# Kernel tuning notes

Measured on AMD Instinct MI355X. Metric: run time of the kernel, lower is better.

Reference implementation:

```python
import jax, jax.numpy as jnp
import numpy as np

NUM_EXPERTS = 8
TOP_K = 2


def setup_inputs() -> dict:
    key = jax.random.key(0)
    k1, k2, k3, k4, k5 = jax.random.split(key, 5)
    B, S, H, F, E = 4, 2048, 1024, 4096, NUM_EXPERTS
    return {
        "hidden_states": jax.random.normal(k1, (B, S, H), dtype=jnp.float32),
        "gate_w": jax.random.normal(k2, (E, H), dtype=jnp.float32) * 0.02,
        "w1": jax.random.normal(k3, (E, F, H), dtype=jnp.float32) * 0.02,
        "w3": jax.random.normal(k4, (E, F, H), dtype=jnp.float32) * 0.02,
        "w2": jax.random.normal(k5, (E, H, F), dtype=jnp.float32) * 0.02,
    }


def reference(hidden_states, gate_w, w1, w3, w2):
    B, S, H = hidden_states.shape
    E = gate_w.shape[0]
    x = hidden_states.reshape(-1, H)  # [T, H]
    T = x.shape[0]

    # Router: logits -> fp32 softmax -> top-k -> renormalize (Mixtral)
    router_logits = x @ gate_w.T  # [T, E]
    probs = jax.nn.softmax(router_logits.astype(jnp.float32), axis=-1)
    top_w, top_idx = jax.lax.top_k(probs, TOP_K)  # [T, K]
    top_w = top_w / jnp.sum(top_w, axis=-1, keepdims=True)
    top_w = top_w.astype(x.dtype)

    # Combine weights per (token, expert); zero for unselected experts.
    comb = jnp.zeros((T, E), dtype=x.dtype).at[
        jnp.arange(T)[:, None], top_idx
    ].add(top_w)  # [T, E]

    out = jnp.zeros((T, H), dtype=x.dtype)
    for e in range(E):  # structural loop over distinct expert weights
        h = jax.nn.silu(x @ w1[e].T) * (x @ w3[e].T)  # [T, F]
        out = out + comb[:, e:e + 1] * (h @ w2[e].T)  # [T, H]

    return out.reshape(B, S, H), router_logits
```

## Files before the change

kernel.cpp:

```cpp
#include <hip/hip_runtime.h>
#include <hip/hip_bf16.h>
#include <stdint.h>

#define T_TOK 8192
#define H_DIM 1024
#define F_DIM 4096
#define NEXP  8
#define CAP        17408
#define CAP_TILES  136

typedef __attribute__((ext_vector_type(8))) short bf16x8;
typedef __attribute__((ext_vector_type(4))) float f32x4;

#define AS1 __attribute__((address_space(1)))
#define AS3 __attribute__((address_space(3)))

__device__ __forceinline__ void gload_lds16(const void* g, void* l) {
  __builtin_amdgcn_global_load_lds((const AS1 void*)g, (AS3 void*)l, 16, 0, 0);
}

struct TK { int i0, i1; float w0, w1; };

__global__ __launch_bounds__(256) void router_kernel(
    const float* __restrict__ x, const float* __restrict__ gw,
    float* __restrict__ logits, int* __restrict__ counts, TK* __restrict__ tk)
{
  const int lane = threadIdx.x & 63;
  const int t = blockIdx.x * 4 + (threadIdx.x >> 6);
  const float* xp = x + (size_t)t * H_DIM;
  float xr[16];
#pragma unroll
  for (int i = 0; i < 16; ++i) xr[i] = xp[lane + i * 64];
  float lg[NEXP];
#pragma unroll
  for (int e = 0; e < NEXP; ++e) {
    const float* gp = gw + e * H_DIM;
    float acc = 0.f;
#pragma unroll
    for (int i = 0; i < 16; ++i) acc += xr[i] * gp[lane + i * 64];
#pragma unroll
    for (int s = 32; s > 0; s >>= 1) acc += __shfl_xor(acc, s, 64);
    lg[e] = acc;
  }
  if (lane < NEXP) logits[(size_t)t * NEXP + lane] = lg[lane];
  if (lane == 0) {
    int i0 = 0; float m0 = lg[0];
#pragma unroll
    for (int e = 1; e < NEXP; ++e) if (lg[e] > m0) { m0 = lg[e]; i0 = e; }
    int i1 = -1; float m1 = -1e30f;
#pragma unroll
    for (int e = 0; e < NEXP; ++e) if (e != i0 && lg[e] > m1) { m1 = lg[e]; i1 = e; }
    float r = expf(m1 - m0);
    float w0 = 1.f / (1.f + r);
    float w1 = r / (1.f + r);
    TK v; v.i0 = i0; v.i1 = i1; v.w0 = w0; v.w1 = w1;
    tk[t] = v;
    atomicAdd(&counts[i0], 1);
    atomicAdd(&counts[i1], 1);
  }
}

__global__ __launch_bounds__(256) void scan_kernel(
    const int* __restrict__ counts, int* __restrict__ offs,
    int* __restrict__ cursor, int* __restrict__ tile_expert)
{
  __shared__ int so[NEXP + 1];
  const int tid = threadIdx.x;
  if (tid == 0) {
    int o = 0;
    for (int e = 0; e < NEXP; ++e) {
      so[e] = o; offs[e] = o; cursor[e] = o;
      o += (counts[e] + 127) & ~127;
    }
    so[NEXP] = o; offs[NEXP] = o;
  }
  __syncthreads();
  for (int ti = tid; ti < CAP_TILES; ti += 256) {
    int row = ti * 128;
    int e = NEXP - 1;
#pragma unroll
    for (int k = 0; k < NEXP; ++k)
      if (row >= so[k] && row < so[k + 1]) { e = k; break; }
    tile_expert[ti] = e;
  }
}

__global__ __launch_bounds__(256) void scatter_kernel(
    const TK* __restrict__ tk, int* __restrict__ cursor,
    int* __restrict__ pair_tok, float* __restrict__ pair_w,
    int2* __restrict__ inv)
{
  int t = blockIdx.x * 256 + threadIdx.x;
  if (t >= T_TOK) return;
  TK v = tk[t];
  int p0 = atomicAdd(&cursor[v.i0], 1);
  pair_tok[p0] = t; pair_w[p0] = v.w0;
  int p1 = atomicAdd(&cursor[v.i1], 1);
  pair_tok[p1] = t; pair_w[p1] = v.w1;
  inv[t] = make_int2(p0, p1);
}

union Pack8 { __hip_bfloat16 o[8]; uint4 u; };

__global__ __launch_bounds__(256) void gather_kernel(
    const float* __restrict__ x, const int* __restrict__ pair_tok,
    __hip_bfloat16* __restrict__ xg)
{
  int idx = blockIdx.x * 256 + threadIdx.x;
  int row = idx >> 7;
  int c8  = (idx & 127) << 3;
  int tok = pair_tok[row];
  const float4* src = reinterpret_cast<const float4*>(x + (size_t)tok * H_DIM + c8);
  float4 a = src[0], b = src[1];
  Pack8 pk;
  pk.o[0] = __float2bfloat16(a.x); pk.o[1] = __float2bfloat16(a.y);
  pk.o[2] = __float2bfloat16(a.z); pk.o[3] = __float2bfloat16(a.w);
  pk.o[4] = __float2bfloat16(b.x); pk.o[5] = __float2bfloat16(b.y);
  pk.o[6] = __float2bfloat16(b.z); pk.o[7] = __float2bfloat16(b.w);
  *reinterpret_cast<uint4*>(xg + (size_t)row * H_DIM + c8) = pk.u;
}

__global__ __launch_bounds__(256) void convert_kernel(
    const float* __restrict__ src, __hip_bfloat16* __restrict__ dst, long long n)
{
  long long i = ((long long)blockIdx.x * 256 + threadIdx.x) * 8;
  if (i >= n) return;
  float4 a = *reinterpret_cast<const float4*>(src + i);
  float4 b = *reinterpret_cast<const float4*>(src + i + 4);
  Pack8 pk;
  pk.o[0] = __float2bfloat16(a.x); pk.o[1] = __float2bfloat16(a.y);
  pk.o[2] = __float2bfloat16(a.z); pk.o[3] = __float2bfloat16(a.w);
  pk.o[4] = __float2bfloat16(b.x); pk.o[5] = __float2bfloat16(b.y);
  pk.o[6] = __float2bfloat16(b.z); pk.o[7] = __float2bfloat16(b.w);
  *reinterpret_cast<uint4*>(dst + i) = pk.u;
}


__global__ __launch_bounds__(256, 2) void gemm1_kernel(
    const __hip_bfloat16* __restrict__ xg,
    const __hip_bfloat16* __restrict__ w1b,
    const __hip_bfloat16* __restrict__ w3b,
    const int* __restrict__ tile_expert,
    __hip_bfloat16* __restrict__ h)
{
  __shared__ __hip_bfloat16 sA[128 * 32], sB1[128 * 32], sB3[128 * 32];
  const int n_ = blockIdx.x;
  const int swz = (n_ & 7) * 544 + (n_ >> 3);
  const int tf = swz & 31;
  const int tm = swz >> 5;
  const int e  = tile_expert[tm];
  const int tid = threadIdx.x;

  const __hip_bfloat16* A  = xg  + (size_t)tm * 128 * H_DIM;
  const __hip_bfloat16* B1 = w1b + (size_t)e * F_DIM * H_DIM + (size_t)tf * 128 * H_DIM;
  const __hip_bfloat16* B3 = w3b + (size_t)e * F_DIM * H_DIM + (size_t)tf * 128 * H_DIM;

  const int r     = tid >> 2;
  const int s_src = (tid & 3) ^ ((r >> 1) & 3);
  const int kc    = s_src * 8;
  const int lo    = tid * 8;

  f32x4 acc1[4][4] = {};
  f32x4 acc3[4][4] = {};

  const int wv = tid >> 6, lane = tid & 63;
  const int wr = wv >> 1, wc = wv & 1;
  const int l16 = lane & 15, lk = lane >> 4;
  const int rdk = (lk * 8) ^ (((l16 >> 1) & 3) * 8);

  for (int kt = 0; kt < H_DIM / 32; ++kt) {
    __syncthreads();
    const int gk = kt * 32 + kc;
    gload_lds16(A  + (size_t)r * H_DIM + gk,          &sA [lo]);
    gload_lds16(A  + (size_t)(r + 64) * H_DIM + gk,   &sA [2048 + lo]);
    gload_lds16(B1 + (size_t)r * H_DIM + gk,          &sB1[lo]);
    gload_lds16(B1 + (size_t)(r + 64) * H_DIM + gk,   &sB1[2048 + lo]);
    gload_lds16(B3 + (size_t)r * H_DIM + gk,          &sB3[lo]);
    gload_lds16(B3 + (size_t)(r + 64) * H_DIM + gk,   &sB3[2048 + lo]);
    __syncthreads();

    bf16x8 af[4], b1f[4], b3f[4];
#pragma unroll
    for (int m = 0; m < 4; ++m)
      af[m] = *reinterpret_cast<const bf16x8*>(&sA[(wr * 64 + m * 16 + l16) * 32 + rdk]);
#pragma unroll
    for (int n = 0; n < 4; ++n) {
      b1f[n] = *reinterpret_cast<const bf16x8*>(&sB1[(wc * 64 + n * 16 + l16) * 32 + rdk]);
      b3f[n] = *reinterpret_cast<const bf16x8*>(&sB3[(wc * 64 + n * 16 + l16) * 32 + rdk]);
    }
#pragma unroll
    for (int m = 0; m < 4; ++m)
#pragma unroll
      for (int n = 0; n < 4; ++n) {
        acc1[m][n] = __builtin_amdgcn_mfma_f32_16x16x32_bf16(af[m], b1f[n], acc1[m][n], 0, 0, 0);
        acc3[m][n] = __builtin_amdgcn_mfma_f32_16x16x32_bf16(af[m], b3f[n], acc3[m][n], 0, 0, 0);
      }
  }

  __hip_bfloat16* hp = h + (size_t)tm * 128 * F_DIM + (size_t)tf * 128;
#pragma unroll
  for (int m = 0; m < 4; ++m)
#pragma unroll
    for (int n = 0; n < 4; ++n)
#pragma unroll
      for (int j = 0; j < 4; ++j) {
        int row = wr * 64 + m * 16 + lk * 4 + j;
        int col = wc * 64 + n * 16 + l16;
        float c1 = acc1[m][n][j];
        float c3 = acc3[m][n][j];
        float s  = c1 / (1.f + expf(-c1));
        hp[(size_t)row * F_DIM + col] = __float2bfloat16(s * c3);
      }
}

__global__ __launch_bounds__(256, 2) void gemm2_kernel(
    const __hip_bfloat16* __restrict__ h,
    const __hip_bfloat16* __restrict__ w2b,
    const int* __restrict__ tile_expert,
    const float* __restrict__ pair_w,
    float* __restrict__ y)
{
  __shared__ __hip_bfloat16 sA[128 * 32], sB[128 * 32];
  const int n_ = blockIdx.x;
  const int swz = (n_ & 7) * 136 + (n_ >> 3);
  const int tn = swz & 7;
  const int tm = swz >> 3;
  const int e  = tile_expert[tm];
  const int tid = threadIdx.x;

  const __hip_bfloat16* A = h   + (size_t)tm * 128 * F_DIM;
  const __hip_bfloat16* B = w2b + (size_t)e * H_DIM * F_DIM + (size_t)tn * 128 * F_DIM;

  const int r     = tid >> 2;
  const int s_src = (tid & 3) ^ ((r >> 1) & 3);
  const int kc    = s_src * 8;
  const int lo    = tid * 8;

  f32x4 acc[4][4] = {};
  const int wv = tid >> 6, lane = tid & 63;
  const int wr = wv >> 1, wc = wv & 1;
  const int l16 = lane & 15, lk = lane >> 4;
  const int rdk = (lk * 8) ^ (((l16 >> 1) & 3) * 8);

  for (int kt = 0; kt < F_DIM / 32; ++kt) {
    __syncthreads();
    const int gk = kt * 32 + kc;
    gload_lds16(A + (size_t)r * F_DIM + gk,          &sA[lo]);
    gload_lds16(A + (size_t)(r + 64) * F_DIM + gk,   &sA[2048 + lo]);
    gload_lds16(B + (size_t)r * F_DIM + gk,          &sB[lo]);
    gload_lds16(B + (size_t)(r + 64) * F_DIM + gk,   &sB[2048 + lo]);
    __syncthreads();

    bf16x8 af[4], bf[4];
#pragma unroll
    for (int m = 0; m < 4; ++m)
      af[m] = *reinterpret_cast<const bf16x8*>(&sA[(wr * 64 + m * 16 + l16) * 32 + rdk]);
#pragma unroll
    for (int n = 0; n < 4; ++n)
      bf[n] = *reinterpret_cast<const bf16x8*>(&sB[(wc * 64 + n * 16 + l16) * 32 + rdk]);
#pragma unroll
    for (int m = 0; m < 4; ++m)
#pragma unroll
      for (int n = 0; n < 4; ++n)
        acc[m][n] = __builtin_amdgcn_mfma_f32_16x16x32_bf16(af[m], bf[n], acc[m][n], 0, 0, 0);
  }

#pragma unroll
  for (int m = 0; m < 4; ++m)
#pragma unroll
    for (int j = 0; j < 4; ++j) {
      int rowg = tm * 128 + wr * 64 + m * 16 + lk * 4 + j;
      float w = pair_w[rowg];
      float* op = y + (size_t)rowg * H_DIM + tn * 128 + wc * 64;
#pragma unroll
      for (int n = 0; n < 4; ++n)
        op[n * 16 + l16] = w * acc[m][n][j];
    }
}

__global__ __launch_bounds__(256) void combine_kernel(
    const float* __restrict__ y, const int2* __restrict__ inv,
    float* __restrict__ out)
{
  int idx = blockIdx.x * 256 + threadIdx.x;
  int t  = idx >> 8;
  int c  = (idx & 255) << 2;
  int2 p = inv[t];
  float4 a = *reinterpret_cast<const float4*>(y + (size_t)p.x * H_DIM + c);
  float4 b = *reinterpret_cast<const float4*>(y + (size_t)p.y * H_DIM + c);
  float4 o; o.x = a.x + b.x; o.y = a.y + b.y; o.z = a.z + b.z; o.w = a.w + b.w;
  *reinterpret_cast<float4*>(out + (size_t)t * H_DIM + c) = o;
}

#define WS_COUNTS   0
#define WS_CURSOR   32
#define WS_OFFS     64
#define WS_TILEEXP  128
#define WS_TK       1024
#define WS_PAIRTOK  132096
#define WS_PAIRW    201728
#define WS_ZERO_BYTES 271360
#define WS_INV      271360
#define WS_XG       336896ll
#define WS_W1       (WS_XG + 35651584ll)
#define WS_W3       (WS_W1 + 67108864ll)
#define WS_W2       (WS_W3 + 67108864ll)
#define WS_H        (WS_W2 + 67108864ll)
#define WS_Y        WS_XG

extern "C" void kernel_launch(void* const* d_in, const int* in_sizes, int n_in,
                              void* d_out, int out_size, void* d_ws, size_t ws_size,
                              hipStream_t stream) {
  const float* x  = (const float*)d_in[0];
  const float* gw = (const float*)d_in[1];
  const float* w1 = (const float*)d_in[2];
  const float* w3 = (const float*)d_in[3];
  const float* w2 = (const float*)d_in[4];
  float* out    = (float*)d_out;
  float* logits = out + (size_t)T_TOK * H_DIM;

  char* ws = (char*)d_ws;
  int*   counts   = (int*)(ws + WS_COUNTS);
  int*   cursor   = (int*)(ws + WS_CURSOR);
  int*   offs     = (int*)(ws + WS_OFFS);
  int*   tile_exp = (int*)(ws + WS_TILEEXP);
  TK*    tk       = (TK*)(ws + WS_TK);
  int*   pair_tok = (int*)(ws + WS_PAIRTOK);
  float* pair_w   = (float*)(ws + WS_PAIRW);
  int2*  inv      = (int2*)(ws + WS_INV);
  __hip_bfloat16* xg  = (__hip_bfloat16*)(ws + WS_XG);
  __hip_bfloat16* w1b = (__hip_bfloat16*)(ws + WS_W1);
  __hip_bfloat16* w3b = (__hip_bfloat16*)(ws + WS_W3);
  __hip_bfloat16* w2b = (__hip_bfloat16*)(ws + WS_W2);
  __hip_bfloat16* hbuf = (__hip_bfloat16*)(ws + WS_H);
  float* ybuf = (float*)(ws + WS_Y);

  hipMemsetAsync(d_ws, 0, WS_ZERO_BYTES, stream);

  const long long nW = (long long)NEXP * F_DIM * H_DIM;
  convert_kernel<<<16384, 256, 0, stream>>>(w1, w1b, nW);
  convert_kernel<<<16384, 256, 0, stream>>>(w3, w3b, nW);
  convert_kernel<<<16384, 256, 0, stream>>>(w2, w2b, nW);

  router_kernel<<<T_TOK / 4, 256, 0, stream>>>(x, gw, logits, counts, tk);
  scan_kernel<<<1, 256, 0, stream>>>(counts, offs, cursor, tile_exp);
  scatter_kernel<<<T_TOK / 256, 256, 0, stream>>>(tk, cursor, pair_tok, pair_w, inv);
  gather_kernel<<<(CAP * 128) / 256, 256, 0, stream>>>(x, pair_tok, xg);

  gemm1_kernel<<<CAP_TILES * (F_DIM / 128), 256, 0, stream>>>(
      xg, w1b, w3b, tile_exp, hbuf);
  gemm2_kernel<<<CAP_TILES * (H_DIM / 128), 256, 0, stream>>>(
      hbuf, w2b, tile_exp, pair_w, ybuf);
  combine_kernel<<<(T_TOK * H_DIM / 4) / 256, 256, 0, stream>>>(ybuf, inv, out);
}
```

Baseline: 1.011 ms.

## Use 256-row tiles, 512 threads, BK=64 double-buffered LDS in expert GEMMs

Both expert GEMMs move to 256x128 tiles with 8 waves, a K-step of 64, and double-buffered LDS. The next tile's global-to-LDS load is issued before the current tile's MFMAs, and s_setprio raises wave priority around the MFMA block. Expert capacity padding becomes 256-row multiples, so there is more padded work, but B reuse per tile doubles and each loop step needs one barrier instead of two. The larger LDS footprint (about 96 KB for gemm1) may limit occupancy.

After: 1.120 ms. 10.8% more time.

```diff
diff --git a/kernel.cpp b/kernel.cpp
--- a/kernel.cpp
+++ b/kernel.cpp
@@ -6,8 +6,8 @@
 #define H_DIM 1024
 #define F_DIM 4096
 #define NEXP  8
-#define CAP        17408
-#define CAP_TILES  136
+#define CAP        18432
+#define CTILES     72
 
 typedef __attribute__((ext_vector_type(8))) short bf16x8;
 typedef __attribute__((ext_vector_type(4))) float f32x4;
@@ -70,13 +70,13 @@
     int o = 0;
     for (int e = 0; e < NEXP; ++e) {
       so[e] = o; offs[e] = o; cursor[e] = o;
-      o += (counts[e] + 127) & ~127;
+      o += (counts[e] + 255) & ~255;
     }
     so[NEXP] = o; offs[NEXP] = o;
   }
   __syncthreads();
-  for (int ti = tid; ti < CAP_TILES; ti += 256) {
-    int row = ti * 128;
+  for (int ti = tid; ti < CTILES; ti += 256) {
+    int row = ti * 256;
     int e = NEXP - 1;
 #pragma unroll
     for (int k = 0; k < NEXP; ++k)
@@ -136,68 +136,101 @@
 }
 
 
-__global__ __launch_bounds__(256, 2) void gemm1_kernel(
+__global__ __launch_bounds__(512, 2) void gemm1_kernel(
     const __hip_bfloat16* __restrict__ xg,
     const __hip_bfloat16* __restrict__ w1b,
     const __hip_bfloat16* __restrict__ w3b,
     const int* __restrict__ tile_expert,
     __hip_bfloat16* __restrict__ h)
 {
-  __shared__ __hip_bfloat16 sA[128 * 32], sB1[128 * 32], sB3[128 * 32];
+  __shared__ __hip_bfloat16 sA[2][256 * 64];
+  __shared__ __hip_bfloat16 sB1[2][128 * 64];
+  __shared__ __hip_bfloat16 sB3[2][128 * 64];
+
   const int n_ = blockIdx.x;
-  const int swz = (n_ & 7) * 544 + (n_ >> 3);
+  const int swz = (n_ & 7) * 288 + (n_ >> 3);
+  const int tm = swz >> 5;
   const int tf = swz & 31;
-  const int tm = swz >> 5;
   const int e  = tile_expert[tm];
   const int tid = threadIdx.x;
 
-  const __hip_bfloat16* A  = xg  + (size_t)tm * 128 * H_DIM;
+  const __hip_bfloat16* A  = xg  + (size_t)tm * 256 * H_DIM;
   const __hip_bfloat16* B1 = w1b + (size_t)e * F_DIM * H_DIM + (size_t)tf * 128 * H_DIM;
   const __hip_bfloat16* B3 = w3b + (size_t)e * F_DIM * H_DIM + (size_t)tf * 128 * H_DIM;
 
-  const int r     = tid >> 2;
-  const int s_src = (tid & 3) ^ ((r >> 1) & 3);
-  const int kc    = s_src * 8;
-  const int lo    = tid * 8;
-
-  f32x4 acc1[4][4] = {};
-  f32x4 acc3[4][4] = {};
+  const int rs    = tid >> 3;
+  const int lslot = (tid & 7) ^ (rs & 7);
+  const int ldst  = tid * 8;
+  const __hip_bfloat16* As  = A  + (size_t)rs * H_DIM + lslot * 8;
+  const __hip_bfloat16* B1s = B1 + (size_t)rs * H_DIM + lslot * 8;
+  const __hip_bfloat16* B3s = B3 + (size_t)rs * H_DIM + lslot * 8;
 
   const int wv = tid >> 6, lane = tid & 63;
   const int wr = wv >> 1, wc = wv & 1;
   const int l16 = lane & 15, lk = lane >> 4;
-  const int rdk = (lk * 8) ^ (((l16 >> 1) & 3) * 8);
-
-  for (int kt = 0; kt < H_DIM / 32; ++kt) {
+  int rowA[4], rowB[4];
+#pragma unroll
+  for (int m = 0; m < 4; ++m) rowA[m] = (wr * 64 + m * 16 + l16) * 64;
+#pragma unroll
+  for (int n = 0; n < 4; ++n) rowB[n] = (wc * 64 + n * 16 + l16) * 64;
+  const int ps[2] = { ((0 + lk) ^ (l16 & 7)) * 8, ((4 + lk) ^ (l16 & 7)) * 8 };
+
+  f32x4 acc1[4][4] = {};
+  f32x4 acc3[4][4] = {};
+
+#pragma unroll
+  for (int c = 0; c < 4; ++c)
+    gload_lds16(As + (size_t)c * 64 * H_DIM, &sA[0][c * 4096 + ldst]);
+#pragma unroll
+  for (int c = 0; c < 2; ++c) {
+    gload_lds16(B1s + (size_t)c * 64 * H_DIM, &sB1[0][c * 4096 + ldst]);
+    gload_lds16(B3s + (size_t)c * 64 * H_DIM, &sB3[0][c * 4096 + ldst]);
+  }
+  __syncthreads();
+
+  int cur = 0;
+  for (int kt = 0; kt < H_DIM / 64; ++kt) {
+    const int nxt = cur ^ 1;
+    if (kt + 1 < H_DIM / 64) {
+      const int gk = (kt + 1) * 64;
+#pragma unroll
+      for (int c = 0; c < 4; ++c)
+        gload_lds16(As + (size_t)c * 64 * H_DIM + gk, &sA[nxt][c * 4096 + ldst]);
+#pragma unroll
+      for (int c = 0; c < 2; ++c) {
+        gload_lds16(B1s + (size_t)c * 64 * H_DIM + gk, &sB1[nxt][c * 4096 + ldst]);
+        gload_lds16(B3s + (size_t)c * 64 * H_DIM + gk, &sB3[nxt][c * 4096 + ldst]);
+      }
+    }
+    const __hip_bfloat16* sAc  = sA[cur];
+    const __hip_bfloat16* sB1c = sB1[cur];
+    const __hip_bfloat16* sB3c = sB3[cur];
+#pragma unroll
+    for (int ks = 0; ks < 2; ++ks) {
+      bf16x8 af[4], b1f[4], b3f[4];
+#pragma unroll
+      for (int m = 0; m < 4; ++m)
+        af[m] = *reinterpret_cast<const bf16x8*>(&sAc[rowA[m] + ps[ks]]);
+#pragma unroll
+      for (int n = 0; n < 4; ++n) {
+        b1f[n] = *reinterpret_cast<const bf16x8*>(&sB1c[rowB[n] + ps[ks]]);
+        b3f[n] = *reinterpret_cast<const bf16x8*>(&sB3c[rowB[n] + ps[ks]]);
+      }
+      __builtin_amdgcn_s_setprio(1);
+#pragma unroll
+      for (int m = 0; m < 4; ++m)
+#pragma unroll
+        for (int n = 0; n < 4; ++n) {
+          acc1[m][n] = __builtin_amdgcn_mfma_f32_16x16x32_bf16(af[m], b1f[n], acc1[m][n], 0, 0, 0);
+          acc3[m][n] = __builtin_amdgcn_mfma_f32_16x16x32_bf16(af[m], b3f[n], acc3[m][n], 0, 0, 0);
+        }
+      __builtin_amdgcn_s_setprio(0);
+    }
     __syncthreads();
-    const int gk = kt * 32 + kc;
-    gload_lds16(A  + (size_t)r * H_DIM + gk,          &sA [lo]);
-    gload_lds16(A  + (size_t)(r + 64) * H_DIM + gk,   &sA [2048 + lo]);
-    gload_lds16(B1 + (size_t)r * H_DIM + gk,          &sB1[lo]);
-    gload_lds16(B1 + (size_t)(r + 64) * H_DIM + gk,   &sB1[2048 + lo]);
-    gload_lds16(B3 + (size_t)r * H_DIM + gk,          &sB3[lo]);
-    gload_lds16(B3 + (size_t)(r + 64) * H_DIM + gk,   &sB3[2048 + lo]);
-    __syncthreads();
-
-    bf16x8 af[4], b1f[4], b3f[4];
-#pragma unroll
-    for (int m = 0; m < 4; ++m)
-      af[m] = *reinterpret_cast<const bf16x8*>(&sA[(wr * 64 + m * 16 + l16) * 32 + rdk]);
-#pragma unroll
-    for (int n = 0; n < 4; ++n) {
-      b1f[n] = *reinterpret_cast<const bf16x8*>(&sB1[(wc * 64 + n * 16 + l16) * 32 + rdk]);
-      b3f[n] = *reinterpret_cast<const bf16x8*>(&sB3[(wc * 64 + n * 16 + l16) * 32 + rdk]);
-    }
-#pragma unroll
-    for (int m = 0; m < 4; ++m)
-#pragma unroll
-      for (int n = 0; n < 4; ++n) {
-        acc1[m][n] = __builtin_amdgcn_mfma_f32_16x16x32_bf16(af[m], b1f[n], acc1[m][n], 0, 0, 0);
-        acc3[m][n] = __builtin_amdgcn_mfma_f32_16x16x32_bf16(af[m], b3f[n], acc3[m][n], 0, 0, 0);
-      }
-  }
-
-  __hip_bfloat16* hp = h + (size_t)tm * 128 * F_DIM + (size_t)tf * 128;
+    cur = nxt;
+  }
+
+  __hip_bfloat16* hp = h + (size_t)tm * 256 * F_DIM + (size_t)tf * 128;
 #pragma unroll
   for (int m = 0; m < 4; ++m)
 #pragma unroll
@@ -213,63 +246,92 @@
       }
 }
 
-__global__ __launch_bounds__(256, 2) void gemm2_kernel(
+__global__ __launch_bounds__(512, 2) void gemm2_kernel(
     const __hip_bfloat16* __restrict__ h,
     const __hip_bfloat16* __restrict__ w2b,
     const int* __restrict__ tile_expert,
     const float* __restrict__ pair_w,
     float* __restrict__ y)
 {
-  __shared__ __hip_bfloat16 sA[128 * 32], sB[128 * 32];
+  __shared__ __hip_bfloat16 sA[2][256 * 64];
+  __shared__ __hip_bfloat16 sB[2][128 * 64];
+
   const int n_ = blockIdx.x;
-  const int swz = (n_ & 7) * 136 + (n_ >> 3);
+  const int swz = (n_ & 7) * 72 + (n_ >> 3);
+  const int tm = swz >> 3;
   const int tn = swz & 7;
-  const int tm = swz >> 3;
   const int e  = tile_expert[tm];
   const int tid = threadIdx.x;
 
-  const __hip_bfloat16* A = h   + (size_t)tm * 128 * F_DIM;
+  const __hip_bfloat16* A = h   + (size_t)tm * 256 * F_DIM;
   const __hip_bfloat16* B = w2b + (size_t)e * H_DIM * F_DIM + (size_t)tn * 128 * F_DIM;
 
-  const int r     = tid >> 2;
-  const int s_src = (tid & 3) ^ ((r >> 1) & 3);
-  const int kc    = s_src * 8;
-  const int lo    = tid * 8;
-
-  f32x4 acc[4][4] = {};
+  const int rs    = tid >> 3;
+  const int lslot = (tid & 7) ^ (rs & 7);
+  const int ldst  = tid * 8;
+  const __hip_bfloat16* As = A + (size_t)rs * F_DIM + lslot * 8;
+  const __hip_bfloat16* Bs = B + (size_t)rs * F_DIM + lslot * 8;
+
   const int wv = tid >> 6, lane = tid & 63;
   const int wr = wv >> 1, wc = wv & 1;
   const int l16 = lane & 15, lk = lane >> 4;
-  const int rdk = (lk * 8) ^ (((l16 >> 1) & 3) * 8);
-
-  for (int kt = 0; kt < F_DIM / 32; ++kt) {
+  int rowA[4], rowB[4];
+#pragma unroll
+  for (int m = 0; m < 4; ++m) rowA[m] = (wr * 64 + m * 16 + l16) * 64;
+#pragma unroll
+  for (int n = 0; n < 4; ++n) rowB[n] = (wc * 64 + n * 16 + l16) * 64;
+  const int ps[2] = { ((0 + lk) ^ (l16 & 7)) * 8, ((4 + lk) ^ (l16 & 7)) * 8 };
+
+  f32x4 acc[4][4] = {};
+
+#pragma unroll
+  for (int c = 0; c < 4; ++c)
+    gload_lds16(As + (size_t)c * 64 * F_DIM, &sA[0][c * 4096 + ldst]);
+#pragma unroll
+  for (int c = 0; c < 2; ++c)
+    gload_lds16(Bs + (size_t)c * 64 * F_DIM, &sB[0][c * 4096 + ldst]);
+  __syncthreads();
+
+  int cur = 0;
+  for (int kt = 0; kt < F_DIM / 64; ++kt) {
+    const int nxt = cur ^ 1;
+    if (kt + 1 < F_DIM / 64) {
+      const int gk = (kt + 1) * 64;
+#pragma unroll
+      for (int c = 0; c < 4; ++c)
+        gload_lds16(As + (size_t)c * 64 * F_DIM + gk, &sA[nxt][c * 4096 + ldst]);
+#pragma unroll
+      for (int c = 0; c < 2; ++c)
+        gload_lds16(Bs + (size_t)c * 64 * F_DIM + gk, &sB[nxt][c * 4096 + ldst]);
+    }
+    const __hip_bfloat16* sAc = sA[cur];
+    const __hip_bfloat16* sBc = sB[cur];
+#pragma unroll
+    for (int ks = 0; ks < 2; ++ks) {
+      bf16x8 af[4], bf[4];
+#pragma unroll
+      for (int m = 0; m < 4; ++m)
+        af[m] = *reinterpret_cast<const bf16x8*>(&sAc[rowA[m] + ps[ks]]);
+#pragma unroll
+      for (int n = 0; n < 4; ++n)
+        bf[n] = *reinterpret_cast<const bf16x8*>(&sBc[rowB[n] + ps[ks]]);
+      __builtin_amdgcn_s_setprio(1);
+#pragma unroll
+      for (int m = 0; m < 4; ++m)
+#pragma unroll
+        for (int n = 0; n < 4; ++n)
+          acc[m][n] = __builtin_amdgcn_mfma_f32_16x16x32_bf16(af[m], bf[n], acc[m][n], 0, 0, 0);
+      __builtin_amdgcn_s_setprio(0);
+    }
     __syncthreads();
-    const int gk = kt * 32 + kc;
-    gload_lds16(A + (size_t)r * F_DIM + gk,          &sA[lo]);
-    gload_lds16(A + (size_t)(r + 64) * F_DIM + gk,   &sA[2048 + lo]);
-    gload_lds16(B + (size_t)r * F_DIM + gk,          &sB[lo]);
-    gload_lds16(B + (size_t)(r + 64) * F_DIM + gk,   &sB[2048 + lo]);
-    __syncthreads();
-
-    bf16x8 af[4], bf[4];
-#pragma unroll
-    for (int m = 0; m < 4; ++m)
-      af[m] = *reinterpret_cast<const bf16x8*>(&sA[(wr * 64 + m * 16 + l16) * 32 + rdk]);
-#pragma unroll
-    for (int n = 0; n < 4; ++n)
-      bf[n] = *reinterpret_cast<const bf16x8*>(&sB[(wc * 64 + n * 16 + l16) * 32 + rdk]);
-#pragma unroll
-    for (int m = 0; m < 4; ++m)
-#pragma unroll
-      for (int n = 0; n < 4; ++n)
-        acc[m][n] = __builtin_amdgcn_mfma_f32_16x16x32_bf16(af[m], bf[n], acc[m][n], 0, 0, 0);
+    cur = nxt;
   }
 
 #pragma unroll
   for (int m = 0; m < 4; ++m)
 #pragma unroll
     for (int j = 0; j < 4; ++j) {
-      int rowg = tm * 128 + wr * 64 + m * 16 + lk * 4 + j;
+      int rowg = tm * 256 + wr * 64 + m * 16 + lk * 4 + j;
       float w = pair_w[rowg];
       float* op = y + (size_t)rowg * H_DIM + tn * 128 + wc * 64;
 #pragma unroll
@@ -298,11 +360,11 @@
 #define WS_TILEEXP  128
 #define WS_TK       1024
 #define WS_PAIRTOK  132096
-#define WS_PAIRW    201728
-#define WS_ZERO_BYTES 271360
-#define WS_INV      271360
-#define WS_XG       336896ll
-#define WS_W1       (WS_XG + 35651584ll)
+#define WS_PAIRW    205824
+#define WS_ZERO_BYTES 279552
+#define WS_INV      279552
+#define WS_XG       345088ll
+#define WS_W1       (WS_XG + 37748736ll)
 #define WS_W3       (WS_W1 + 67108864ll)
 #define WS_W2       (WS_W3 + 67108864ll)
 #define WS_H        (WS_W2 + 67108864ll)
@@ -347,9 +409,9 @@
   scatter_kernel<<<T_TOK / 256, 256, 0, stream>>>(tk, cursor, pair_tok, pair_w, inv);
   gather_kernel<<<(CAP * 128) / 256, 256, 0, stream>>>(x, pair_tok, xg);
 
-  gemm1_kernel<<<CAP_TILES * (F_DIM / 128), 256, 0, stream>>>(
+  gemm1_kernel<<<CTILES * (F_DIM / 128), 512, 0, stream>>>(
       xg, w1b, w3b, tile_exp, hbuf);
-  gemm2_kernel<<<CAP_TILES * (H_DIM / 128), 256, 0, stream>>>(
+  gemm2_kernel<<<CTILES * (H_DIM / 128), 512, 0, stream>>>(
       hbuf, w2b, tile_exp, pair_w, ybuf);
   combine_kernel<<<(T_TOK * H_DIM / 4) / 256, 256, 0, stream>>>(ybuf, inv, out);
 }
```

## Rewrite expert GEMMs with larger tiles, double-buffered LDS and interleaved load/MMA schedule

Applied to the files above, without the earlier changes.

Both grouped GEMMs move to 512-thread blocks with bigger tiles: 256x(128+128) for gemm1 and 128x256 for gemm2, with BK=64. Each uses two LDS buffers, so the global-to-LDS loads for the next K step are split into quarters and overlapped with MFMA phases. This relies on explicit vmcnt waits, raw s_barrier and s_setprio in place of the old load-sync-compute loop. Expert segments are now padded to 256 rows, which raises the capacity and padding work and means the workspace offsets have to be changed too.

After: 1.233 ms. 1.22x slower.

```diff
diff --git a/kernel.cpp b/kernel.cpp
--- a/kernel.cpp
+++ b/kernel.cpp
@@ -6,8 +6,8 @@
 #define H_DIM 1024
 #define F_DIM 4096
 #define NEXP  8
-#define CAP        17408
-#define CAP_TILES  136
+#define CAP        18432
+#define CTILES     72
 
 typedef __attribute__((ext_vector_type(8))) short bf16x8;
 typedef __attribute__((ext_vector_type(4))) float f32x4;
@@ -18,6 +18,11 @@
 __device__ __forceinline__ void gload_lds16(const void* g, void* l) {
   __builtin_amdgcn_global_load_lds((const AS1 void*)g, (AS3 void*)l, 16, 0, 0);
 }
+
+#define WAIT_VMCNT(n) asm volatile("s_waitcnt vmcnt(" #n ")" ::: "memory")
+#define SBAR  do { __builtin_amdgcn_sched_barrier(0); __builtin_amdgcn_s_barrier(); } while (0)
+#define PRIO1 __builtin_amdgcn_s_setprio(1)
+#define PRIO0 __builtin_amdgcn_s_setprio(0)
 
 struct TK { int i0, i1; float w0, w1; };
 
@@ -70,13 +75,13 @@
     int o = 0;
     for (int e = 0; e < NEXP; ++e) {
       so[e] = o; offs[e] = o; cursor[e] = o;
-      o += (counts[e] + 127) & ~127;
+      o += (counts[e] + 255) & ~255;
     }
     so[NEXP] = o; offs[NEXP] = o;
   }
   __syncthreads();
-  for (int ti = tid; ti < CAP_TILES; ti += 256) {
-    int row = ti * 128;
+  for (int ti = tid; ti < CTILES; ti += 256) {
+    int row = ti * 256;
     int e = NEXP - 1;
 #pragma unroll
     for (int k = 0; k < NEXP; ++k)
@@ -136,146 +141,201 @@
 }
 
 
-__global__ __launch_bounds__(256, 2) void gemm1_kernel(
+__global__ __launch_bounds__(512, 2) void gemm1_kernel(
     const __hip_bfloat16* __restrict__ xg,
     const __hip_bfloat16* __restrict__ w1b,
     const __hip_bfloat16* __restrict__ w3b,
     const int* __restrict__ tile_expert,
     __hip_bfloat16* __restrict__ h)
 {
-  __shared__ __hip_bfloat16 sA[128 * 32], sB1[128 * 32], sB3[128 * 32];
+  __shared__ __hip_bfloat16 sA[2][256 * 64];
+  __shared__ __hip_bfloat16 sB[2][256 * 64];
+
   const int n_ = blockIdx.x;
-  const int swz = (n_ & 7) * 544 + (n_ >> 3);
-  const int tf = swz & 31;
-  const int tm = swz >> 5;
+  const int x_ = (n_ & 7) * 288 + (n_ >> 3);
+  const int tm = x_ >> 5;
+  const int tf = x_ & 31;
   const int e  = tile_expert[tm];
   const int tid = threadIdx.x;
 
-  const __hip_bfloat16* A  = xg  + (size_t)tm * 128 * H_DIM;
+  const __hip_bfloat16* A  = xg  + (size_t)tm * 256 * H_DIM;
   const __hip_bfloat16* B1 = w1b + (size_t)e * F_DIM * H_DIM + (size_t)tf * 128 * H_DIM;
   const __hip_bfloat16* B3 = w3b + (size_t)e * F_DIM * H_DIM + (size_t)tf * 128 * H_DIM;
 
-  const int r     = tid >> 2;
-  const int s_src = (tid & 3) ^ ((r >> 1) & 3);
-  const int kc    = s_src * 8;
-  const int lo    = tid * 8;
-
-  f32x4 acc1[4][4] = {};
-  f32x4 acc3[4][4] = {};
+  const int rs  = tid >> 3;
+  const int sl  = tid & 7;
+  const int xsl = (sl ^ (rs & 7)) * 8;
 
   const int wv = tid >> 6, lane = tid & 63;
-  const int wr = wv >> 1, wc = wv & 1;
+  const int wm = wv >> 2, wn = wv & 3;
   const int l16 = lane & 15, lk = lane >> 4;
-  const int rdk = (lk * 8) ^ (((l16 >> 1) & 3) * 8);
-
-  for (int kt = 0; kt < H_DIM / 32; ++kt) {
-    __syncthreads();
-    const int gk = kt * 32 + kc;
-    gload_lds16(A  + (size_t)r * H_DIM + gk,          &sA [lo]);
-    gload_lds16(A  + (size_t)(r + 64) * H_DIM + gk,   &sA [2048 + lo]);
-    gload_lds16(B1 + (size_t)r * H_DIM + gk,          &sB1[lo]);
-    gload_lds16(B1 + (size_t)(r + 64) * H_DIM + gk,   &sB1[2048 + lo]);
-    gload_lds16(B3 + (size_t)r * H_DIM + gk,          &sB3[lo]);
-    gload_lds16(B3 + (size_t)(r + 64) * H_DIM + gk,   &sB3[2048 + lo]);
-    __syncthreads();
-
-    bf16x8 af[4], b1f[4], b3f[4];
-#pragma unroll
-    for (int m = 0; m < 4; ++m)
-      af[m] = *reinterpret_cast<const bf16x8*>(&sA[(wr * 64 + m * 16 + l16) * 32 + rdk]);
-#pragma unroll
-    for (int n = 0; n < 4; ++n) {
-      b1f[n] = *reinterpret_cast<const bf16x8*>(&sB1[(wc * 64 + n * 16 + l16) * 32 + rdk]);
-      b3f[n] = *reinterpret_cast<const bf16x8*>(&sB3[(wc * 64 + n * 16 + l16) * 32 + rdk]);
-    }
-#pragma unroll
-    for (int m = 0; m < 4; ++m)
-#pragma unroll
-      for (int n = 0; n < 4; ++n) {
-        acc1[m][n] = __builtin_amdgcn_mfma_f32_16x16x32_bf16(af[m], b1f[n], acc1[m][n], 0, 0, 0);
-        acc3[m][n] = __builtin_amdgcn_mfma_f32_16x16x32_bf16(af[m], b3f[n], acc3[m][n], 0, 0, 0);
-      }
-  }
-
-  __hip_bfloat16* hp = h + (size_t)tm * 128 * F_DIM + (size_t)tf * 128;
-#pragma unroll
-  for (int m = 0; m < 4; ++m)
-#pragma unroll
-    for (int n = 0; n < 4; ++n)
+  const int ps0 = ((0 + lk) ^ (l16 & 7)) * 8;
+  const int ps1 = ((4 + lk) ^ (l16 & 7)) * 8;
+
+  f32x4 acc1[8][2] = {};
+  f32x4 acc3[8][2] = {};
+  bf16x8 a[4][2], b[2][2];
+
+#define G1_ST_A0(bb, gg) { \
+    gload_lds16(A + (size_t)rs * H_DIM + (gg) + xsl,         &sA[bb][rs * 64 + sl * 8]); \
+    gload_lds16(A + (size_t)(128 + rs) * H_DIM + (gg) + xsl, &sA[bb][(128 + rs) * 64 + sl * 8]); }
+#define G1_ST_A1(bb, gg) { \
+    gload_lds16(A + (size_t)(64 + rs) * H_DIM + (gg) + xsl,  &sA[bb][(64 + rs) * 64 + sl * 8]); \
+    gload_lds16(A + (size_t)(192 + rs) * H_DIM + (gg) + xsl, &sA[bb][(192 + rs) * 64 + sl * 8]); }
+#define G1_ST_B0(bb, gg) { \
+    gload_lds16(B1 + (size_t)rs * H_DIM + (gg) + xsl,        &sB[bb][rs * 64 + sl * 8]); \
+    gload_lds16(B1 + (size_t)(64 + rs) * H_DIM + (gg) + xsl, &sB[bb][(64 + rs) * 64 + sl * 8]); }
+#define G1_ST_B1(bb, gg) { \
+    gload_lds16(B3 + (size_t)rs * H_DIM + (gg) + xsl,        &sB[bb][(128 + rs) * 64 + sl * 8]); \
+    gload_lds16(B3 + (size_t)(64 + rs) * H_DIM + (gg) + xsl, &sB[bb][(192 + rs) * 64 + sl * 8]); }
+#define G1_RD_A(mh) { \
+    _Pragma("unroll") for (int f2 = 0; f2 < 4; ++f2) { \
+      int ro = (wm * 128 + ((mh) * 4 + f2) * 16 + l16) * 64; \
+      a[f2][0] = *reinterpret_cast<const bf16x8*>(&sA[cur][ro + ps0]); \
+      a[f2][1] = *reinterpret_cast<const bf16x8*>(&sA[cur][ro + ps1]); } }
+#define G1_RD_B(nh) { \
+    _Pragma("unroll") for (int nf = 0; nf < 2; ++nf) { \
+      int ro = ((nh) * 128 + wn * 32 + nf * 16 + l16) * 64; \
+      b[nf][0] = *reinterpret_cast<const bf16x8*>(&sB[cur][ro + ps0]); \
+      b[nf][1] = *reinterpret_cast<const bf16x8*>(&sB[cur][ro + ps1]); } }
+#define G1_MMA(ACC, mh) { PRIO1; \
+    _Pragma("unroll") for (int f2 = 0; f2 < 4; ++f2) \
+    _Pragma("unroll") for (int nf = 0; nf < 2; ++nf) { \
+      ACC[(mh) * 4 + f2][nf] = __builtin_amdgcn_mfma_f32_16x16x32_bf16(a[f2][0], b[nf][0], ACC[(mh) * 4 + f2][nf], 0, 0, 0); \
+      ACC[(mh) * 4 + f2][nf] = __builtin_amdgcn_mfma_f32_16x16x32_bf16(a[f2][1], b[nf][1], ACC[(mh) * 4 + f2][nf], 0, 0, 0); } \
+    PRIO0; }
+
+  G1_ST_A0(0, 0); G1_ST_B0(0, 0); G1_ST_A1(0, 0); G1_ST_B1(0, 0);
+  WAIT_VMCNT(0); SBAR;
+
+  for (int t = 0; t < 16; ++t) {
+    const int cur = t & 1, nb = cur ^ 1;
+    const int gg = (t < 15 ? t + 1 : 15) * 64;
+    G1_ST_A0(nb, gg); WAIT_VMCNT(6);
+    G1_RD_A(0); G1_RD_B(0); G1_MMA(acc1, 0); SBAR;
+    G1_ST_B0(nb, gg); WAIT_VMCNT(6);
+    G1_RD_A(1); G1_MMA(acc1, 1); SBAR;
+    G1_ST_A1(nb, gg); WAIT_VMCNT(6);
+    G1_RD_B(1); G1_MMA(acc3, 1); SBAR;
+    G1_ST_B1(nb, gg); WAIT_VMCNT(6);
+    G1_RD_A(0); G1_MMA(acc3, 0); SBAR;
+  }
+
+  __hip_bfloat16* hp = h + (size_t)tm * 256 * F_DIM + (size_t)tf * 128;
+#pragma unroll
+  for (int f = 0; f < 8; ++f)
+#pragma unroll
+    for (int nf = 0; nf < 2; ++nf)
 #pragma unroll
       for (int j = 0; j < 4; ++j) {
-        int row = wr * 64 + m * 16 + lk * 4 + j;
-        int col = wc * 64 + n * 16 + l16;
-        float c1 = acc1[m][n][j];
-        float c3 = acc3[m][n][j];
+        int row = wm * 128 + f * 16 + lk * 4 + j;
+        int col = wn * 32 + nf * 16 + l16;
+        float c1 = acc1[f][nf][j];
+        float c3 = acc3[f][nf][j];
         float s  = c1 / (1.f + expf(-c1));
         hp[(size_t)row * F_DIM + col] = __float2bfloat16(s * c3);
       }
-}
-
-__global__ __launch_bounds__(256, 2) void gemm2_kernel(
+#undef G1_ST_A0
+#undef G1_ST_A1
+#undef G1_ST_B0
+#undef G1_ST_B1
+#undef G1_RD_A
+#undef G1_RD_B
+#undef G1_MMA
+}
+
+__global__ __launch_bounds__(512, 2) void gemm2_kernel(
     const __hip_bfloat16* __restrict__ h,
     const __hip_bfloat16* __restrict__ w2b,
     const int* __restrict__ tile_expert,
     const float* __restrict__ pair_w,
     float* __restrict__ y)
 {
-  __shared__ __hip_bfloat16 sA[128 * 32], sB[128 * 32];
+  __shared__ __hip_bfloat16 sA[2][128 * 64];
+  __shared__ __hip_bfloat16 sB[2][256 * 64];
+
   const int n_ = blockIdx.x;
-  const int swz = (n_ & 7) * 136 + (n_ >> 3);
-  const int tn = swz & 7;
-  const int tm = swz >> 3;
-  const int e  = tile_expert[tm];
+  const int x_ = (n_ & 7) * 72 + (n_ >> 3);
+  const int tn = x_ / 144;
+  const int tm = x_ % 144;
+  const int e  = tile_expert[tm >> 1];
   const int tid = threadIdx.x;
 
   const __hip_bfloat16* A = h   + (size_t)tm * 128 * F_DIM;
-  const __hip_bfloat16* B = w2b + (size_t)e * H_DIM * F_DIM + (size_t)tn * 128 * F_DIM;
-
-  const int r     = tid >> 2;
-  const int s_src = (tid & 3) ^ ((r >> 1) & 3);
-  const int kc    = s_src * 8;
-  const int lo    = tid * 8;
+  const __hip_bfloat16* B = w2b + (size_t)e * H_DIM * F_DIM + (size_t)tn * 256 * F_DIM;
+
+  const int rs  = tid >> 3;
+  const int sl  = tid & 7;
+  const int xsl = (sl ^ (rs & 7)) * 8;
+  const int rb  = (rs >> 5) * 64 + (rs & 31);
+
+  const int wv = tid >> 6, lane = tid & 63;
+  const int wm = wv >> 2, wn = wv & 3;
+  const int l16 = lane & 15, lk = lane >> 4;
+  const int ps0 = ((0 + lk) ^ (l16 & 7)) * 8;
+  const int ps1 = ((4 + lk) ^ (l16 & 7)) * 8;
 
   f32x4 acc[4][4] = {};
-  const int wv = tid >> 6, lane = tid & 63;
-  const int wr = wv >> 1, wc = wv & 1;
-  const int l16 = lane & 15, lk = lane >> 4;
-  const int rdk = (lk * 8) ^ (((l16 >> 1) & 3) * 8);
-
-  for (int kt = 0; kt < F_DIM / 32; ++kt) {
-    __syncthreads();
-    const int gk = kt * 32 + kc;
-    gload_lds16(A + (size_t)r * F_DIM + gk,          &sA[lo]);
-    gload_lds16(A + (size_t)(r + 64) * F_DIM + gk,   &sA[2048 + lo]);
-    gload_lds16(B + (size_t)r * F_DIM + gk,          &sB[lo]);
-    gload_lds16(B + (size_t)(r + 64) * F_DIM + gk,   &sB[2048 + lo]);
-    __syncthreads();
-
-    bf16x8 af[4], bf[4];
-#pragma unroll
-    for (int m = 0; m < 4; ++m)
-      af[m] = *reinterpret_cast<const bf16x8*>(&sA[(wr * 64 + m * 16 + l16) * 32 + rdk]);
-#pragma unroll
-    for (int n = 0; n < 4; ++n)
-      bf[n] = *reinterpret_cast<const bf16x8*>(&sB[(wc * 64 + n * 16 + l16) * 32 + rdk]);
-#pragma unroll
-    for (int m = 0; m < 4; ++m)
-#pragma unroll
-      for (int n = 0; n < 4; ++n)
-        acc[m][n] = __builtin_amdgcn_mfma_f32_16x16x32_bf16(af[m], bf[n], acc[m][n], 0, 0, 0);
-  }
-
-#pragma unroll
-  for (int m = 0; m < 4; ++m)
+  bf16x8 a[2][2], b[2][2];
+
+#define G2_ST_A(bb, gg) { \
+    gload_lds16(A + (size_t)rs * F_DIM + (gg) + xsl,        &sA[bb][rs * 64 + sl * 8]); \
+    gload_lds16(A + (size_t)(64 + rs) * F_DIM + (gg) + xsl, &sA[bb][(64 + rs) * 64 + sl * 8]); }
+#define G2_ST_B0(bb, gg) { \
+    gload_lds16(B + (size_t)rb * F_DIM + (gg) + xsl,          &sB[bb][rb * 64 + sl * 8]); \
+    gload_lds16(B + (size_t)(128 + rb) * F_DIM + (gg) + xsl,  &sB[bb][(128 + rb) * 64 + sl * 8]); }
+#define G2_ST_B1(bb, gg) { \
+    gload_lds16(B + (size_t)(32 + rb) * F_DIM + (gg) + xsl,   &sB[bb][(32 + rb) * 64 + sl * 8]); \
+    gload_lds16(B + (size_t)(160 + rb) * F_DIM + (gg) + xsl,  &sB[bb][(160 + rb) * 64 + sl * 8]); }
+#define G2_RD_A(mh) { \
+    _Pragma("unroll") for (int f2 = 0; f2 < 2; ++f2) { \
+      int ro = (wm * 64 + ((mh) * 2 + f2) * 16 + l16) * 64; \
+      a[f2][0] = *reinterpret_cast<const bf16x8*>(&sA[cur][ro + ps0]); \
+      a[f2][1] = *reinterpret_cast<const bf16x8*>(&sA[cur][ro + ps1]); } }
+#define G2_RD_B(nh) { \
+    _Pragma("unroll") for (int nf = 0; nf < 2; ++nf) { \
+      int ro = (wn * 64 + (nh) * 32 + nf * 16 + l16) * 64; \
+      b[nf][0] = *reinterpret_cast<const bf16x8*>(&sB[cur][ro + ps0]); \
+      b[nf][1] = *reinterpret_cast<const bf16x8*>(&sB[cur][ro + ps1]); } }
+#define G2_MMA(mh, nh) { PRIO1; \
+    _Pragma("unroll") for (int f2 = 0; f2 < 2; ++f2) \
+    _Pragma("unroll") for (int nf = 0; nf < 2; ++nf) { \
+      acc[(mh) * 2 + f2][(nh) * 2 + nf] = __builtin_amdgcn_mfma_f32_16x16x32_bf16(a[f2][0], b[nf][0], acc[(mh) * 2 + f2][(nh) * 2 + nf], 0, 0, 0); \
+      acc[(mh) * 2 + f2][(nh) * 2 + nf] = __builtin_amdgcn_mfma_f32_16x16x32_bf16(a[f2][1], b[nf][1], acc[(mh) * 2 + f2][(nh) * 2 + nf], 0, 0, 0); } \
+    PRIO0; }
+
+  G2_ST_A(0, 0); G2_ST_B0(0, 0); G2_ST_B1(0, 0);
+  WAIT_VMCNT(0); SBAR;
+
+  for (int t = 0; t < 64; ++t) {
+    const int cur = t & 1, nb = cur ^ 1;
+    const int gg = (t < 63 ? t + 1 : 63) * 64;
+    G2_ST_A(nb, gg); WAIT_VMCNT(4);
+    G2_RD_A(0); G2_RD_B(0); G2_MMA(0, 0); SBAR;
+    G2_ST_B0(nb, gg);
+    G2_RD_A(1); G2_MMA(1, 0); SBAR;
+    G2_ST_B1(nb, gg); WAIT_VMCNT(6);
+    G2_RD_B(1); G2_MMA(1, 1); SBAR;
+    G2_RD_A(0); G2_MMA(0, 1); SBAR;
+  }
+
+#pragma unroll
+  for (int f = 0; f < 4; ++f)
 #pragma unroll
     for (int j = 0; j < 4; ++j) {
-      int rowg = tm * 128 + wr * 64 + m * 16 + lk * 4 + j;
+      int rowg = tm * 128 + wm * 64 + f * 16 + lk * 4 + j;
       float w = pair_w[rowg];
-      float* op = y + (size_t)rowg * H_DIM + tn * 128 + wc * 64;
-#pragma unroll
-      for (int n = 0; n < 4; ++n)
-        op[n * 16 + l16] = w * acc[m][n][j];
+      float* op = y + (size_t)rowg * H_DIM + tn * 256 + wn * 64;
+#pragma unroll
+      for (int nf = 0; nf < 4; ++nf)
+        op[nf * 16 + l16] = w * acc[f][nf][j];
     }
+#undef G2_ST_A
+#undef G2_ST_B0
+#undef G2_ST_B1
+#undef G2_RD_A
+#undef G2_RD_B
+#undef G2_MMA
 }
 
 __global__ __launch_bounds__(256) void combine_kernel(
@@ -298,11 +358,11 @@
 #define WS_TILEEXP  128
 #define WS_TK       1024
 #define WS_PAIRTOK  132096
-#define WS_PAIRW    201728
-#define WS_ZERO_BYTES 271360
-#define WS_INV      271360
-#define WS_XG       336896ll
-#define WS_W1       (WS_XG + 35651584ll)
+#define WS_PAIRW    205824
+#define WS_ZERO_BYTES 279552
+#define WS_INV      279552
+#define WS_XG       345088ll
+#define WS_W1       (WS_XG + 37748736ll)
 #define WS_W3       (WS_W1 + 67108864ll)
 #define WS_W2       (WS_W3 + 67108864ll)
 #define WS_H        (WS_W2 + 67108864ll)
@@ -347,9 +407,9 @@
   scatter_kernel<<<T_TOK / 256, 256, 0, stream>>>(tk, cursor, pair_tok, pair_w, inv);
   gather_kernel<<<(CAP * 128) / 256, 256, 0, stream>>>(x, pair_tok, xg);
 
-  gemm1_kernel<<<CAP_TILES * (F_DIM / 128), 256, 0, stream>>>(
+  gemm1_kernel<<<CTILES * (F_DIM / 128), 512, 0, stream>>>(
       xg, w1b, w3b, tile_exp, hbuf);
-  gemm2_kernel<<<CAP_TILES * (H_DIM / 128), 256, 0, stream>>>(
+  gemm2_kernel<<<(CAP / 128) * (H_DIM / 256), 512, 0, stream>>>(
       hbuf, w2b, tile_exp, pair_w, ybuf);
   combine_kernel<<<(T_TOK * H_DIM / 4) / 256, 256, 0, stream>>>(ybuf, inv, out);
 }
```
